# Performance work log

Hardware: AMD Instinct MI355X
Metric: run time of the kernel (lower is better)

## Reference

```python
import jax, jax.numpy as jnp
import numpy as np

HEADS = 8

def setup_inputs() -> dict:
    key = jax.random.key(0)
    ks = jax.random.split(key, 11)
    B, S, E = 4, 2048, 512
    sc = 1.0 / np.sqrt(E)
    return {
        "inputs": jax.random.normal(ks[0], (B, S, E), jnp.float32),
        "entangle": jax.random.uniform(ks[1], (S,), jnp.float32),
        "Wq": jax.random.normal(ks[2], (E, E), jnp.float32) * sc,
        "bq": jax.random.normal(ks[3], (E,), jnp.float32) * 0.01,
        "Wk": jax.random.normal(ks[4], (E, E), jnp.float32) * sc,
        "bk": jax.random.normal(ks[5], (E,), jnp.float32) * 0.01,
        "Wv": jax.random.normal(ks[6], (E, E), jnp.float32) * sc,
        "bv": jax.random.normal(ks[7], (E,), jnp.float32) * 0.01,
        "Wo": jax.random.normal(ks[8], (E, E), jnp.float32) * sc,
        "bo": jax.random.normal(ks[9], (E,), jnp.float32) * 0.01,
    }

def reference(inputs, entangle, Wq, bq, Wk, bk, Wv, bv, Wo, bo):
    B, S, E = inputs.shape
    H = HEADS
    D = E // H
    # torch nn.Linear: y = x @ W.T + b
    Q = (inputs @ Wq.T + bq).reshape(B, S, H, D)
    K = (inputs @ Wk.T + bk).reshape(B, S, H, D)
    V = (inputs @ Wv.T + bv).reshape(B, S, H, D)
    scores = jnp.einsum('bqhd,bkhd->bhqk', Q, K) / jnp.sqrt(jnp.float32(D))
    # entangle broadcast as (1,1,S,1): per-query-position scaling before softmax
    scores = scores * entangle[None, None, :, None]
    attn = jax.nn.softmax(scores, axis=-1)
    out = jnp.einsum('bhqk,bkhd->bqhd', attn, V).reshape(B, S, E)
    return out @ Wo.T + bo
```

## Files before the change

### kernel.cpp

```cpp
#include <hip/hip_runtime.h>
#include <hip/hip_bf16.h>

#define BB 4
#define SS 2048
#define EE 512
#define HH 8
#define DD 64

typedef __attribute__((ext_vector_type(8))) short bf16x8;
typedef __attribute__((ext_vector_type(4))) float f32x4;
typedef __attribute__((ext_vector_type(4))) unsigned int u32x4;

__device__ __forceinline__ unsigned short f2bf(float f) {
    __hip_bfloat16 h = __float2bfloat16(f);
    return *reinterpret_cast<unsigned short*>(&h);
}

__device__ __forceinline__ unsigned int cvtpk(float lo, float hi) {
    unsigned int r;
    asm("v_cvt_pk_bf16_f32 %0, %1, %2" : "=v"(r) : "v"(lo), "v"(hi));
    return r;
}

__device__ __forceinline__ float ex2(float x) {
    float r;
    asm("v_exp_f32 %0, %1" : "=v"(r) : "v"(x));
    return r;
}

__device__ __forceinline__ void pl32(unsigned int& a, unsigned int& b) {
    asm("v_permlane32_swap_b32 %0, %1" : "+v"(a), "+v"(b));
}
__device__ __forceinline__ void pl16(unsigned int& a, unsigned int& b) {
    asm("v_permlane16_swap_b32 %0, %1" : "+v"(a), "+v"(b));
}

__device__ __forceinline__ void gll16(const unsigned short* g, unsigned short* l) {
    __builtin_amdgcn_global_load_lds(
        (const __attribute__((address_space(1))) unsigned int*)g,
        (__attribute__((address_space(3))) unsigned int*)l,
        16, 0, 0);
}

template<typename OutT, bool TRANSPOSE_V, int TM, bool AF32>
__global__ __launch_bounds__(256, 3)
void gemm_mfma_nt(const unsigned short* __restrict__ Abf,
                  const float* __restrict__ Af,
                  const float* __restrict__ W0, const float* __restrict__ b0, OutT* __restrict__ C0,
                  const float* __restrict__ W1, const float* __restrict__ b1, OutT* __restrict__ C1,
                  const float* __restrict__ W2, const float* __restrict__ b2, OutT* __restrict__ C2,
                  const float* __restrict__ rowscale,
                  int M, int N, int K)
{
    const float* W    = (blockIdx.z == 0) ? W0 : (blockIdx.z == 1) ? W1 : W2;
    const float* bias = (blockIdx.z == 0) ? b0 : (blockIdx.z == 1) ? b1 : b2;
    OutT* C           = (blockIdx.z == 0) ? C0 : (blockIdx.z == 1) ? C1 : C2;

    constexpr int MT  = TM / 32;
    constexpr int NA  = TM / 64;
    constexpr int STG = 3 * TM * 32;
    __shared__ unsigned short lds[STG + 3 * 128 * 32];
    unsigned short* As = lds;
    unsigned short* Bs = lds + STG;

    const int tid  = threadIdx.x;
    const int wave = tid >> 6, lane = tid & 63;
    const int quad = lane >> 4, r16 = lane & 15;
    const int m0 = blockIdx.x * TM, n0 = blockIdx.y * 128;
    const int wm0 = (wave >> 1) * (TM / 2), wn0 = (wave & 1) * 64;

    f32x4 acc[MT][4];
    const f32x4 zero = {0.f, 0.f, 0.f, 0.f};
    #pragma unroll
    for (int i = 0; i < MT; ++i)
        #pragma unroll
        for (int j = 0; j < 4; ++j) acc[i][j] = zero;

    const int swz = (r16 >> 1) & 3;

    int acb[NA > 0 ? NA : 1], arow[NA > 0 ? NA : 1], acc_[NA > 0 ? NA : 1];
    #pragma unroll
    for (int j = 0; j < NA; ++j) {
        const int cb = wave * 64 + j * 256, c = cb + lane;
        acb[j] = cb; arow[j] = c >> 2; acc_[j] = (c & 3) ^ ((arow[j] >> 1) & 3);
    }
    int wcb[2], wrow[2], wcc[2];
    #pragma unroll
    for (int j = 0; j < 2; ++j) {
        const int cb = wave * 64 + j * 256, c = cb + lane;
        wcb[j] = cb; wrow[j] = c >> 2; wcc[j] = (c & 3) ^ ((wrow[j] >> 1) & 3);
    }

    f32x4 ra[2 * (NA > 0 ? NA : 1)];
    f32x4 rw[4];

    auto issue = [&](int bi, int k0) {
        if constexpr (AF32) {
            #pragma unroll
            for (int j = 0; j < NA; ++j) {
                const float* p = &Af[(size_t)(m0 + arow[j]) * K + k0 + acc_[j] * 8];
                ra[2 * j]     = *reinterpret_cast<const f32x4*>(p);
                ra[2 * j + 1] = *reinterpret_cast<const f32x4*>(p + 4);
            }
        } else {
            #pragma unroll
            for (int j = 0; j < NA; ++j)
                gll16(&Abf[(size_t)(m0 + arow[j]) * K + k0 + acc_[j] * 8],
                      &As[bi * TM * 32 + acb[j] * 8]);
        }
        #pragma unroll
        for (int j = 0; j < 2; ++j) {
            const float* p = &W[(size_t)(n0 + wrow[j]) * K + k0 + wcc[j] * 8];
            rw[2 * j]     = *reinterpret_cast<const f32x4*>(p);
            rw[2 * j + 1] = *reinterpret_cast<const f32x4*>(p + 4);
        }
    };
    auto commit = [&](int bi) {
        if constexpr (AF32) {
            #pragma unroll
            for (int j = 0; j < NA; ++j) {
                const u32x4 v = {cvtpk(ra[2*j][0], ra[2*j][1]), cvtpk(ra[2*j][2], ra[2*j][3]),
                                 cvtpk(ra[2*j+1][0], ra[2*j+1][1]), cvtpk(ra[2*j+1][2], ra[2*j+1][3])};
                *reinterpret_cast<u32x4*>(&As[bi * TM * 32 + (acb[j] + lane) * 8]) = v;
            }
        }
        #pragma unroll
        for (int j = 0; j < 2; ++j) {
            const u32x4 v = {cvtpk(rw[2*j][0], rw[2*j][1]), cvtpk(rw[2*j][2], rw[2*j][3]),
                             cvtpk(rw[2*j+1][0], rw[2*j+1][1]), cvtpk(rw[2*j+1][2], rw[2*j+1][3])};
            *reinterpret_cast<u32x4*>(&Bs[bi * 128 * 32 + (wcb[j] + lane) * 8]) = v;
        }
    };

    issue(0, 0);
    asm volatile("s_waitcnt vmcnt(0)" ::: "memory");
    commit(0);
    issue(1, 32);

    const int NI = K / 32;
    for (int i = 0; i < NI; ++i) {
        const int cur = i % 3;
        asm volatile("s_waitcnt lgkmcnt(0)" ::: "memory");
        __builtin_amdgcn_s_barrier();
        __builtin_amdgcn_sched_barrier(0);
        if (i + 1 < NI) {
            asm volatile("s_waitcnt vmcnt(0)" ::: "memory");
            commit((i + 1) % 3);
        }
        if (i + 2 < NI) issue((i + 2) % 3, (i + 2) * 32);

        bf16x8 af[MT], bfr[4];
        #pragma unroll
        for (int t = 0; t < MT; ++t)
            af[t]  = *reinterpret_cast<bf16x8*>(&As[cur * TM * 32 + ((wm0 + t * 16 + r16) * 4 + (quad ^ swz)) * 8]);
        #pragma unroll
        for (int t = 0; t < 4; ++t)
            bfr[t] = *reinterpret_cast<bf16x8*>(&Bs[cur * 128 * 32 + ((wn0 + t * 16 + r16) * 4 + (quad ^ swz)) * 8]);
        #pragma unroll
        for (int mt = 0; mt < MT; ++mt)
            #pragma unroll
            for (int nt = 0; nt < 4; ++nt)
                acc[mt][nt] = __builtin_amdgcn_mfma_f32_16x16x32_bf16(
                    af[mt], bfr[nt], acc[mt][nt], 0, 0, 0);
    }

    if (TRANSPOSE_V && blockIdx.z == 2) {
        __syncthreads();
        #pragma unroll
        for (int mt = 0; mt < MT; ++mt) {
            const int s_local = wm0 + mt * 16 + quad * 4;
            #pragma unroll
            for (int nt = 0; nt < 4; ++nt) {
                const int d_local = wn0 + nt * 16 + r16;
                const float bv = bias[n0 + d_local];
                uint2 o;
                o.x = cvtpk(acc[mt][nt][0] + bv, acc[mt][nt][1] + bv);
                o.y = cvtpk(acc[mt][nt][2] + bv, acc[mt][nt][3] + bv);
                *reinterpret_cast<uint2*>(&lds[d_local * 132 + s_local]) = o;
            }
        }
        __syncthreads();
        const int bb = m0 >> 11, s0 = m0 & (SS - 1);
        unsigned short* Vtp = (unsigned short*)C2 + (size_t)bb * EE * SS + s0;
        const int scol = (tid & 15) * 8;
        #pragma unroll
        for (int p = 0; p < 8; ++p) {
            const int row = p * 16 + (tid >> 4);
            const uint2 lo = *reinterpret_cast<const uint2*>(&lds[row * 132 + scol]);
            const uint2 hi = *reinterpret_cast<const uint2*>(&lds[row * 132 + scol + 4]);
            const u32x4 v = {lo.x, lo.y, hi.x, hi.y};
            *reinterpret_cast<u32x4*>(&Vtp[(size_t)(n0 + row) * SS + scol]) = v;
        }
        return;
    }
    if constexpr (sizeof(OutT) == 2) {
        const bool doscale = (rowscale != nullptr) && (blockIdx.z == 0);
        __syncthreads();
        #pragma unroll
        for (int mt = 0; mt < MT; ++mt) {
            float rs[4];
            #pragma unroll
            for (int r = 0; r < 4; ++r) {
                const int row = m0 + wm0 + mt * 16 + quad * 4 + r;
                rs[r] = doscale ? rowscale[row & (SS - 1)] * 0.18033688f : 1.0f;
            }
            #pragma unroll
            for (int nt = 0; nt < 4; ++nt) {
                const int col = wn0 + nt * 16 + r16;
                const float bv = bias[n0 + col];
                #pragma unroll
                for (int r = 0; r < 4; ++r) {
                    const int row = wm0 + mt * 16 + quad * 4 + r;
                    lds[row * 132 + col] = f2bf((acc[mt][nt][r] + bv) * rs[r]);
                }
            }
        }
        __syncthreads();
        const int scol = (tid & 15) * 8;
        #pragma unroll
        for (int p = 0; p < TM / 16; ++p) {
            const int row = p * 16 + (tid >> 4);
            const uint2 lo = *reinterpret_cast<const uint2*>(&lds[row * 132 + scol]);
            const uint2 hi = *reinterpret_cast<const uint2*>(&lds[row * 132 + scol + 4]);
            const u32x4 v = {lo.x, lo.y, hi.x, hi.y};
            *reinterpret_cast<u32x4*>(&((unsigned short*)C)[(size_t)(m0 + row) * N + n0 + scol]) = v;
        }
    } else {
        float* fl = reinterpret_cast<float*>(lds);
        __syncthreads();
        #pragma unroll
        for (int mt = 0; mt < MT; ++mt) {
            #pragma unroll
            for (int nt = 0; nt < 4; ++nt) {
                const int col = wn0 + nt * 16 + r16;
                const float bv = bias[n0 + col];
                #pragma unroll
                for (int r = 0; r < 4; ++r) {
                    const int row = wm0 + mt * 16 + quad * 4 + r;
                    fl[row * 132 + col] = acc[mt][nt][r] + bv;
                }
            }
        }
        __syncthreads();
        const int scol = (tid & 31) * 4;
        #pragma unroll
        for (int p = 0; p < TM / 8; ++p) {
            const int row = p * 8 + (tid >> 5);
            const f32x4 v = *reinterpret_cast<const f32x4*>(&fl[row * 132 + scol]);
            *reinterpret_cast<f32x4*>(&((float*)C)[(size_t)(m0 + row) * N + n0 + scol]) = v;
        }
    }
}

#define QBLK 128
#define KVB  128

__global__ __launch_bounds__(256, 2)
void attn_mfma(const unsigned short* __restrict__ Q,
               const unsigned short* __restrict__ K,
               const unsigned short* __restrict__ Vt,
               unsigned short* __restrict__ O)
{
    __shared__ unsigned short Ks[2][KVB * 64];
    __shared__ unsigned short Vs[2][64 * KVB];

    const int tid  = threadIdx.x;
    const int wave = tid >> 6, lane = tid & 63;
    const int quad = lane >> 4, r16 = lane & 15;
    const int h  = blockIdx.x;
    const int q0 = blockIdx.y * QBLK;
    const int b  = blockIdx.z;
    const size_t base    = (size_t)b * SS * EE + (size_t)h * DD;
    const size_t base_vt = ((size_t)b * HH + h) * DD * SS;

    bf16x8 qf[2][2];
    #pragma unroll
    for (int s = 0; s < 2; ++s) {
        const int qrow = q0 + s * 64 + wave * 16 + r16;
        #pragma unroll
        for (int dh = 0; dh < 2; ++dh)
            qf[s][dh] = *reinterpret_cast<const bf16x8*>(
                &Q[base + (size_t)qrow * EE + dh * 32 + quad * 8]);
    }

    const unsigned short* kp[4];
    const unsigned short* vp[4];
    int cbs[4];
    #pragma unroll
    for (int j = 0; j < 4; ++j) {
        const int cb = wave * 64 + j * 256;
        cbs[j] = cb;
        const int c  = cb + lane;
        const int rowK = c >> 3, ccK = (c & 7) ^ (rowK & 7);
        kp[j] = &K[base + (size_t)rowK * EE + ccK * 8];
        const int rowV = c >> 4, ccV = (c & 15) ^ (rowV & 15);
        vp[j] = &Vt[base_vt + (size_t)rowV * SS + ccV * 8];
    }

    auto stage = [&](int bi, int kt) {
        const size_t ko = (size_t)kt * KVB * EE;
        const int    vo = kt * KVB;
        #pragma unroll
        for (int j = 0; j < 4; ++j) {
            gll16(kp[j] + ko, &Ks[bi][cbs[j] * 8]);
            gll16(vp[j] + vo, &Vs[bi][cbs[j] * 8]);
        }
    };

    float l_lane[2] = {0.f, 0.f};
    f32x4 o_acc[2][4];
    const f32x4 zero = {0.f, 0.f, 0.f, 0.f};
    #pragma unroll
    for (int s = 0; s < 2; ++s)
        #pragma unroll
        for (int dt = 0; dt < 4; ++dt) o_acc[s][dt] = zero;

    const int swz7 = r16 & 7;

    stage(0, 0);

    constexpr int NT = SS / KVB;
    for (int kt = 0; kt < NT; ++kt) {
        const int cur = kt & 1;
        asm volatile("s_waitcnt vmcnt(0)" ::: "memory");
        __builtin_amdgcn_s_barrier();
        __builtin_amdgcn_sched_barrier(0);
        if (kt + 1 < NT) stage(cur ^ 1, kt + 1);

        const unsigned short* Kc = &Ks[cur][0];
        const unsigned short* Vc = &Vs[cur][0];

        f32x4 st[2][8];
        #pragma unroll
        for (int s = 0; s < 2; ++s)
            #pragma unroll
            for (int tn = 0; tn < 8; ++tn) st[s][tn] = zero;
        __builtin_amdgcn_s_setprio(1);
        #pragma unroll
        for (int tn = 0; tn < 8; ++tn) {
            const bf16x8 kf0 = *reinterpret_cast<const bf16x8*>(
                &Kc[((tn * 16 + r16) * 8 + (quad ^ swz7)) * 8]);
            const bf16x8 kf1 = *reinterpret_cast<const bf16x8*>(
                &Kc[((tn * 16 + r16) * 8 + ((quad + 4) ^ swz7)) * 8]);
            #pragma unroll
            for (int s = 0; s < 2; ++s) {
                st[s][tn] = __builtin_amdgcn_mfma_f32_16x16x32_bf16(kf0, qf[s][0], st[s][tn], 0, 0, 0);
                st[s][tn] = __builtin_amdgcn_mfma_f32_16x16x32_bf16(kf1, qf[s][1], st[s][tn], 0, 0, 0);
            }
        }
        __builtin_amdgcn_s_setprio(0);

        bf16x8 pf[2][4];
        #pragma unroll
        for (int s = 0; s < 2; ++s) {
            unsigned int w[8][2];
            #pragma unroll
            for (int tn = 0; tn < 8; ++tn) {
                const float p0 = ex2(st[s][tn][0]);
                const float p1 = ex2(st[s][tn][1]);
                const float p2 = ex2(st[s][tn][2]);
                const float p3 = ex2(st[s][tn][3]);
                l_lane[s] += (p0 + p1) + (p2 + p3);
                w[tn][0] = cvtpk(p0, p1);
                w[tn][1] = cvtpk(p2, p3);
            }
            #pragma unroll
            for (int j = 0; j < 4; ++j) {
                unsigned int a0 = w[2 * j][0], a2 = w[2 * j + 1][0];
                pl32(a0, a2); pl16(a0, a2);
                unsigned int a1 = w[2 * j][1], a3 = w[2 * j + 1][1];
                pl32(a1, a3); pl16(a1, a3);
                const u32x4 u = {a0, a1, a2, a3};
                pf[s][j] = __builtin_bit_cast(bf16x8, u);
            }
        }

        __builtin_amdgcn_s_setprio(1);
        #pragma unroll
        for (int j = 0; j < 4; ++j) {
            #pragma unroll
            for (int dt = 0; dt < 4; ++dt) {
                const bf16x8 vf = *reinterpret_cast<const bf16x8*>(
                    &Vc[((dt * 16 + r16) * 16 + ((4 * j + quad) ^ r16)) * 8]);
                o_acc[0][dt] = __builtin_amdgcn_mfma_f32_16x16x32_bf16(pf[0][j], vf, o_acc[0][dt], 0, 0, 0);
                o_acc[1][dt] = __builtin_amdgcn_mfma_f32_16x16x32_bf16(pf[1][j], vf, o_acc[1][dt], 0, 0, 0);
            }
        }
        __builtin_amdgcn_s_setprio(0);
    }

    float lq[2];
    #pragma unroll
    for (int s = 0; s < 2; ++s) {
        float l = l_lane[s];
        l += __shfl_xor(l, 16, 64);
        l += __shfl_xor(l, 32, 64);
        lq[s] = l;
    }

    unsigned short* ob = &Ks[0][0];
    __syncthreads();
    #pragma unroll
    for (int s = 0; s < 2; ++s) {
        #pragma unroll
        for (int r = 0; r < 4; ++r) {
            const float il = 1.0f / __shfl(lq[s], quad * 4 + r, 64);
            const int ql = s * 64 + wave * 16 + quad * 4 + r;
            #pragma unroll
            for (int dt = 0; dt < 4; ++dt)
                ob[ql * 68 + dt * 16 + r16] = f2bf(o_acc[s][dt][r] * il);
        }
    }
    __syncthreads();
    const int orow = tid >> 3, ocol = (tid & 7) * 8;
    #pragma unroll
    for (int p = 0; p < 4; ++p) {
        const int ql = p * 32 + orow;
        const uint2 lo = *reinterpret_cast<const uint2*>(&ob[ql * 68 + ocol]);
        const uint2 hi = *reinterpret_cast<const uint2*>(&ob[ql * 68 + ocol + 4]);
        const u32x4 v = {lo.x, lo.y, hi.x, hi.y};
        *reinterpret_cast<u32x4*>(&O[base + (size_t)(q0 + ql) * EE + ocol]) = v;
    }
}

extern "C" void kernel_launch(void* const* d_in, const int* in_sizes, int n_in,
                              void* d_out, int out_size, void* d_ws, size_t ws_size,
                              hipStream_t stream) {
    const float* x   = (const float*)d_in[0];
    const float* ent = (const float*)d_in[1];
    const float* Wq  = (const float*)d_in[2];
    const float* bq  = (const float*)d_in[3];
    const float* Wk  = (const float*)d_in[4];
    const float* bk  = (const float*)d_in[5];
    const float* Wv  = (const float*)d_in[6];
    const float* bv  = (const float*)d_in[7];
    const float* Wo  = (const float*)d_in[8];
    const float* bo  = (const float*)d_in[9];
    float* out = (float*)d_out;

    const size_t n_x = (size_t)BB * SS * EE;
    const size_t n_w = (size_t)EE * EE;

    unsigned short* xb  = (unsigned short*)d_ws;
    unsigned short* wqb = xb + n_x;
    unsigned short* wkb = wqb + n_w;
    unsigned short* wvb = wkb + n_w;
    unsigned short* wob = wvb + n_w;
    unsigned short* Qb  = wob + n_w;
    unsigned short* Kb  = Qb + n_x;
    unsigned short* Vtb = Kb + n_x;
    unsigned short* AOb = Vtb + n_x;

    const int M = BB * SS;

    dim3 gq(M / 128, EE / 128, 3);
    gemm_mfma_nt<unsigned short, true, 128, true><<<gq, 256, 0, stream>>>(
        nullptr, x, Wq, bq, Qb, Wk, bk, Kb, Wv, bv, Vtb, ent, M, EE, EE);

    dim3 ga(HH, SS / QBLK, BB);
    attn_mfma<<<ga, 256, 0, stream>>>(Qb, Kb, Vtb, AOb);

    dim3 go(M / 64, EE / 128, 1);
    gemm_mfma_nt<float, false, 64, false><<<go, 256, 0, stream>>>(
        AOb, nullptr, Wo, bo, out, Wo, bo, out, Wo, bo, out, nullptr, M, EE, EE);
}
```

Measured before the change: 156.2 us.

## Fuse Q/K/V projections into one kernel sharing the x tile

Replaces the z-batched QKV GEMM, which used 128-row tiles and reloaded and converted the fp32 input once per projection, with a dedicated kernel. Each block loads a 64-row x tile once and computes all three projections against it, using double buffering. The goal is to cut input reads and fp32-to-bf16 conversions by three times. In exchange, each thread holds three times as many accumulators, which raises register pressure and risks occupancy. The output GEMM is specialised into a simpler non-templated kernel.

```diff
diff --git a/kernel.cpp b/kernel.cpp
--- a/kernel.cpp
+++ b/kernel.cpp
@@ -42,22 +42,190 @@
         16, 0, 0);
 }
 
-template<typename OutT, bool TRANSPOSE_V, int TM, bool AF32>
+__global__ __launch_bounds__(256, 2)
+void qkv_fused(const float* __restrict__ x,
+               const float* __restrict__ Wq, const float* __restrict__ bq, unsigned short* __restrict__ Qb,
+               const float* __restrict__ Wk, const float* __restrict__ bk, unsigned short* __restrict__ Kb,
+               const float* __restrict__ Wv, const float* __restrict__ bv, unsigned short* __restrict__ Vtb,
+               const float* __restrict__ ent)
+{
+    constexpr int K   = EE;
+    constexpr int N   = EE;
+    constexpr int ASZ = 64 * 32;
+    constexpr int BSZ = 128 * 32;
+    constexpr int BUF = ASZ + 3 * BSZ;
+    __shared__ unsigned short lds[2 * BUF];
+
+    const int tid  = threadIdx.x;
+    const int wave = tid >> 6, lane = tid & 63;
+    const int quad = lane >> 4, r16 = lane & 15;
+    const int m0 = blockIdx.x * 64, n0 = blockIdx.y * 128;
+    const int wm0 = (wave >> 1) * 32, wn0 = (wave & 1) * 64;
+
+    const float* Ws[3] = {Wq, Wk, Wv};
+
+    f32x4 acc[3][2][4];
+    const f32x4 zero = {0.f, 0.f, 0.f, 0.f};
+    #pragma unroll
+    for (int o = 0; o < 3; ++o)
+        #pragma unroll
+        for (int mt = 0; mt < 2; ++mt)
+            #pragma unroll
+            for (int nt = 0; nt < 4; ++nt) acc[o][mt][nt] = zero;
+
+    const int swz = (r16 >> 1) & 3;
+
+    const int cbA = wave * 64, cA = cbA + lane;
+    const int rowA = cA >> 2, ccA = (cA & 3) ^ ((rowA >> 1) & 3);
+    int wcb[2], wrow[2], wcc[2];
+    #pragma unroll
+    for (int j = 0; j < 2; ++j) {
+        const int cb = wave * 64 + j * 256, c = cb + lane;
+        wcb[j] = cb; wrow[j] = c >> 2; wcc[j] = (c & 3) ^ ((wrow[j] >> 1) & 3);
+    }
+
+    f32x4 ra[2];
+    f32x4 rw[3][2][2];
+
+    auto issue = [&](int k0) {
+        const float* pa = &x[(size_t)(m0 + rowA) * K + k0 + ccA * 8];
+        ra[0] = *reinterpret_cast<const f32x4*>(pa);
+        ra[1] = *reinterpret_cast<const f32x4*>(pa + 4);
+        #pragma unroll
+        for (int o = 0; o < 3; ++o)
+            #pragma unroll
+            for (int j = 0; j < 2; ++j) {
+                const float* p = &Ws[o][(size_t)(n0 + wrow[j]) * K + k0 + wcc[j] * 8];
+                rw[o][j][0] = *reinterpret_cast<const f32x4*>(p);
+                rw[o][j][1] = *reinterpret_cast<const f32x4*>(p + 4);
+            }
+    };
+    auto commit = [&](int bi) {
+        unsigned short* As = lds + bi * BUF;
+        const u32x4 va = {cvtpk(ra[0][0], ra[0][1]), cvtpk(ra[0][2], ra[0][3]),
+                          cvtpk(ra[1][0], ra[1][1]), cvtpk(ra[1][2], ra[1][3])};
+        *reinterpret_cast<u32x4*>(&As[(cbA + lane) * 8]) = va;
+        #pragma unroll
+        for (int o = 0; o < 3; ++o) {
+            unsigned short* Bo = lds + bi * BUF + ASZ + o * BSZ;
+            #pragma unroll
+            for (int j = 0; j < 2; ++j) {
+                const u32x4 v = {cvtpk(rw[o][j][0][0], rw[o][j][0][1]), cvtpk(rw[o][j][0][2], rw[o][j][0][3]),
+                                 cvtpk(rw[o][j][1][0], rw[o][j][1][1]), cvtpk(rw[o][j][1][2], rw[o][j][1][3])};
+                *reinterpret_cast<u32x4*>(&Bo[(wcb[j] + lane) * 8]) = v;
+            }
+        }
+    };
+
+    issue(0);
+    asm volatile("s_waitcnt vmcnt(0)" ::: "memory");
+    commit(0);
+    issue(32);
+
+    constexpr int NI = K / 32;
+    for (int i = 0; i < NI; ++i) {
+        const int cur = i & 1;
+        asm volatile("s_waitcnt lgkmcnt(0)" ::: "memory");
+        __builtin_amdgcn_s_barrier();
+        __builtin_amdgcn_sched_barrier(0);
+        if (i + 1 < NI) {
+            asm volatile("s_waitcnt vmcnt(0)" ::: "memory");
+            commit(cur ^ 1);
+        }
+        if (i + 2 < NI) issue((i + 2) * 32);
+
+        const unsigned short* As = lds + cur * BUF;
+        bf16x8 af[2];
+        #pragma unroll
+        for (int t = 0; t < 2; ++t)
+            af[t] = *reinterpret_cast<const bf16x8*>(
+                &As[((wm0 + t * 16 + r16) * 4 + (quad ^ swz)) * 8]);
+        #pragma unroll
+        for (int o = 0; o < 3; ++o) {
+            const unsigned short* Bo = lds + cur * BUF + ASZ + o * BSZ;
+            bf16x8 bfr[4];
+            #pragma unroll
+            for (int t = 0; t < 4; ++t)
+                bfr[t] = *reinterpret_cast<const bf16x8*>(
+                    &Bo[((wn0 + t * 16 + r16) * 4 + (quad ^ swz)) * 8]);
+            #pragma unroll
+            for (int mt = 0; mt < 2; ++mt)
+                #pragma unroll
+                for (int nt = 0; nt < 4; ++nt)
+                    acc[o][mt][nt] = __builtin_amdgcn_mfma_f32_16x16x32_bf16(
+                        af[mt], bfr[nt], acc[o][mt][nt], 0, 0, 0);
+        }
+    }
+
+    #pragma unroll
+    for (int o = 0; o < 2; ++o) {
+        const float* bias = (o == 0) ? bq : bk;
+        unsigned short* dst = (o == 0) ? Qb : Kb;
+        __syncthreads();
+        #pragma unroll
+        for (int mt = 0; mt < 2; ++mt) {
+            float rs[4];
+            #pragma unroll
+            for (int r = 0; r < 4; ++r) {
+                const int grow = m0 + wm0 + mt * 16 + quad * 4 + r;
+                rs[r] = (o == 0) ? ent[grow & (SS - 1)] * 0.18033688f : 1.0f;
+            }
+            #pragma unroll
+            for (int nt = 0; nt < 4; ++nt) {
+                const int col = wn0 + nt * 16 + r16;
+                const float bvv = bias[n0 + col];
+                #pragma unroll
+                for (int r = 0; r < 4; ++r) {
+                    const int row = wm0 + mt * 16 + quad * 4 + r;
+                    lds[row * 132 + col] = f2bf((acc[o][mt][nt][r] + bvv) * rs[r]);
+                }
+            }
+        }
+        __syncthreads();
+        const int scol = (tid & 15) * 8;
+        #pragma unroll
+        for (int p = 0; p < 4; ++p) {
+            const int row = p * 16 + (tid >> 4);
+            const uint2 lo = *reinterpret_cast<const uint2*>(&lds[row * 132 + scol]);
+            const uint2 hi = *reinterpret_cast<const uint2*>(&lds[row * 132 + scol + 4]);
+            const u32x4 v = {lo.x, lo.y, hi.x, hi.y};
+            *reinterpret_cast<u32x4*>(&dst[(size_t)(m0 + row) * N + n0 + scol]) = v;
+        }
+    }
+    __syncthreads();
+    #pragma unroll
+    for (int mt = 0; mt < 2; ++mt) {
+        const int s_local = wm0 + mt * 16 + quad * 4;
+        #pragma unroll
+        for (int nt = 0; nt < 4; ++nt) {
+            const int d_local = wn0 + nt * 16 + r16;
+            const float bvv = bv[n0 + d_local];
+            uint2 o2;
+            o2.x = cvtpk(acc[2][mt][nt][0] + bvv, acc[2][mt][nt][1] + bvv);
+            o2.y = cvtpk(acc[2][mt][nt][2] + bvv, acc[2][mt][nt][3] + bvv);
+            *reinterpret_cast<uint2*>(&lds[d_local * 68 + s_local]) = o2;
+        }
+    }
+    __syncthreads();
+    const int bb = m0 >> 11, s0 = m0 & (SS - 1);
+    unsigned short* Vtp = Vtb + (size_t)bb * EE * SS + s0;
+    const int ocol = (tid & 7) * 8;
+    #pragma unroll
+    for (int p = 0; p < 4; ++p) {
+        const int d = p * 32 + (tid >> 3);
+        const uint2 lo = *reinterpret_cast<const uint2*>(&lds[d * 68 + ocol]);
+        const uint2 hi = *reinterpret_cast<const uint2*>(&lds[d * 68 + ocol + 4]);
+        const u32x4 v = {lo.x, lo.y, hi.x, hi.y};
+        *reinterpret_cast<u32x4*>(&Vtp[(size_t)(n0 + d) * SS + ocol]) = v;
+    }
+}
+
 __global__ __launch_bounds__(256, 3)
-void gemm_mfma_nt(const unsigned short* __restrict__ Abf,
-                  const float* __restrict__ Af,
-                  const float* __restrict__ W0, const float* __restrict__ b0, OutT* __restrict__ C0,
-                  const float* __restrict__ W1, const float* __restrict__ b1, OutT* __restrict__ C1,
-                  const float* __restrict__ W2, const float* __restrict__ b2, OutT* __restrict__ C2,
-                  const float* __restrict__ rowscale,
-                  int M, int N, int K)
+void gemm_out(const unsigned short* __restrict__ Abf,
+              const float* __restrict__ W, const float* __restrict__ bias,
+              float* __restrict__ C, int M, int N, int K)
 {
-    const float* W    = (blockIdx.z == 0) ? W0 : (blockIdx.z == 1) ? W1 : W2;
-    const float* bias = (blockIdx.z == 0) ? b0 : (blockIdx.z == 1) ? b1 : b2;
-    OutT* C           = (blockIdx.z == 0) ? C0 : (blockIdx.z == 1) ? C1 : C2;
-
-    constexpr int MT  = TM / 32;
-    constexpr int NA  = TM / 64;
+    constexpr int TM = 64;
     constexpr int STG = 3 * TM * 32;
     __shared__ unsigned short lds[STG + 3 * 128 * 32];
     unsigned short* As = lds;
@@ -69,45 +237,27 @@
     const int m0 = blockIdx.x * TM, n0 = blockIdx.y * 128;
     const int wm0 = (wave >> 1) * (TM / 2), wn0 = (wave & 1) * 64;
 
-    f32x4 acc[MT][4];
+    f32x4 acc[2][4];
     const f32x4 zero = {0.f, 0.f, 0.f, 0.f};
     #pragma unroll
-    for (int i = 0; i < MT; ++i)
+    for (int i = 0; i < 2; ++i)
         #pragma unroll
         for (int j = 0; j < 4; ++j) acc[i][j] = zero;
 
     const int swz = (r16 >> 1) & 3;
 
-    int acb[NA > 0 ? NA : 1], arow[NA > 0 ? NA : 1], acc_[NA > 0 ? NA : 1];
-    #pragma unroll
-    for (int j = 0; j < NA; ++j) {
-        const int cb = wave * 64 + j * 256, c = cb + lane;
-        acb[j] = cb; arow[j] = c >> 2; acc_[j] = (c & 3) ^ ((arow[j] >> 1) & 3);
-    }
+    const int cbA = wave * 64, cA = cbA + lane;
+    const int rowA = cA >> 2, ccA = (cA & 3) ^ ((rowA >> 1) & 3);
     int wcb[2], wrow[2], wcc[2];
     #pragma unroll
     for (int j = 0; j < 2; ++j) {
         const int cb = wave * 64 + j * 256, c = cb + lane;
         wcb[j] = cb; wrow[j] = c >> 2; wcc[j] = (c & 3) ^ ((wrow[j] >> 1) & 3);
     }
-
-    f32x4 ra[2 * (NA > 0 ? NA : 1)];
     f32x4 rw[4];
 
     auto issue = [&](int bi, int k0) {
-        if constexpr (AF32) {
-            #pragma unroll
-            for (int j = 0; j < NA; ++j) {
-                const float* p = &Af[(size_t)(m0 + arow[j]) * K + k0 + acc_[j] * 8];
-                ra[2 * j]     = *reinterpret_cast<const f32x4*>(p);
-                ra[2 * j + 1] = *reinterpret_cast<const f32x4*>(p + 4);
-            }
-        } else {
-            #pragma unroll
-            for (int j = 0; j < NA; ++j)
-                gll16(&Abf[(size_t)(m0 + arow[j]) * K + k0 + acc_[j] * 8],
-                      &As[bi * TM * 32 + acb[j] * 8]);
-        }
+        gll16(&Abf[(size_t)(m0 + rowA) * K + k0 + ccA * 8], &As[bi * TM * 32 + cbA * 8]);
         #pragma unroll
         for (int j = 0; j < 2; ++j) {
             const float* p = &W[(size_t)(n0 + wrow[j]) * K + k0 + wcc[j] * 8];
@@ -116,14 +266,6 @@
         }
     };
     auto commit = [&](int bi) {
-        if constexpr (AF32) {
-            #pragma unroll
-            for (int j = 0; j < NA; ++j) {
-                const u32x4 v = {cvtpk(ra[2*j][0], ra[2*j][1]), cvtpk(ra[2*j][2], ra[2*j][3]),
-                                 cvtpk(ra[2*j+1][0], ra[2*j+1][1]), cvtpk(ra[2*j+1][2], ra[2*j+1][3])};
-                *reinterpret_cast<u32x4*>(&As[bi * TM * 32 + (acb[j] + lane) * 8]) = v;
-            }
-        }
         #pragma unroll
         for (int j = 0; j < 2; ++j) {
             const u32x4 v = {cvtpk(rw[2*j][0], rw[2*j][1]), cvtpk(rw[2*j][2], rw[2*j][3]),
@@ -149,106 +291,43 @@
         }
         if (i + 2 < NI) issue((i + 2) % 3, (i + 2) * 32);
 
-        bf16x8 af[MT], bfr[4];
-        #pragma unroll
-        for (int t = 0; t < MT; ++t)
+        bf16x8 af[2], bfr[4];
+        #pragma unroll
+        for (int t = 0; t < 2; ++t)
             af[t]  = *reinterpret_cast<bf16x8*>(&As[cur * TM * 32 + ((wm0 + t * 16 + r16) * 4 + (quad ^ swz)) * 8]);
         #pragma unroll
         for (int t = 0; t < 4; ++t)
             bfr[t] = *reinterpret_cast<bf16x8*>(&Bs[cur * 128 * 32 + ((wn0 + t * 16 + r16) * 4 + (quad ^ swz)) * 8]);
         #pragma unroll
-        for (int mt = 0; mt < MT; ++mt)
+        for (int mt = 0; mt < 2; ++mt)
             #pragma unroll
             for (int nt = 0; nt < 4; ++nt)
                 acc[mt][nt] = __builtin_amdgcn_mfma_f32_16x16x32_bf16(
                     af[mt], bfr[nt], acc[mt][nt], 0, 0, 0);
     }
 
-    if (TRANSPOSE_V && blockIdx.z == 2) {
-        __syncthreads();
-        #pragma unroll
-        for (int mt = 0; mt < MT; ++mt) {
-            const int s_local = wm0 + mt * 16 + quad * 4;
-            #pragma unroll
-            for (int nt = 0; nt < 4; ++nt) {
-                const int d_local = wn0 + nt * 16 + r16;
-                const float bv = bias[n0 + d_local];
-                uint2 o;
-                o.x = cvtpk(acc[mt][nt][0] + bv, acc[mt][nt][1] + bv);
-                o.y = cvtpk(acc[mt][nt][2] + bv, acc[mt][nt][3] + bv);
-                *reinterpret_cast<uint2*>(&lds[d_local * 132 + s_local]) = o;
-            }
-        }
-        __syncthreads();
-        const int bb = m0 >> 11, s0 = m0 & (SS - 1);
-        unsigned short* Vtp = (unsigned short*)C2 + (size_t)bb * EE * SS + s0;
-        const int scol = (tid & 15) * 8;
-        #pragma unroll
-        for (int p = 0; p < 8; ++p) {
-            const int row = p * 16 + (tid >> 4);
-            const uint2 lo = *reinterpret_cast<const uint2*>(&lds[row * 132 + scol]);
-            const uint2 hi = *reinterpret_cast<const uint2*>(&lds[row * 132 + scol + 4]);
-            const u32x4 v = {lo.x, lo.y, hi.x, hi.y};
-            *reinterpret_cast<u32x4*>(&Vtp[(size_t)(n0 + row) * SS + scol]) = v;
-        }
-        return;
-    }
-    if constexpr (sizeof(OutT) == 2) {
-        const bool doscale = (rowscale != nullptr) && (blockIdx.z == 0);
-        __syncthreads();
-        #pragma unroll
-        for (int mt = 0; mt < MT; ++mt) {
-            float rs[4];
+    float* fl = reinterpret_cast<float*>(lds);
+    __syncthreads();
+    #pragma unroll
+    for (int mt = 0; mt < 2; ++mt) {
+        #pragma unroll
+        for (int nt = 0; nt < 4; ++nt) {
+            const int col = wn0 + nt * 16 + r16;
+            const float bvv = bias[n0 + col];
             #pragma unroll
             for (int r = 0; r < 4; ++r) {
-                const int row = m0 + wm0 + mt * 16 + quad * 4 + r;
-                rs[r] = doscale ? rowscale[row & (SS - 1)] * 0.18033688f : 1.0f;
-            }
-            #pragma unroll
-            for (int nt = 0; nt < 4; ++nt) {
-                const int col = wn0 + nt * 16 + r16;
-                const float bv = bias[n0 + col];
-                #pragma unroll
-                for (int r = 0; r < 4; ++r) {
-                    const int row = wm0 + mt * 16 + quad * 4 + r;
-                    lds[row * 132 + col] = f2bf((acc[mt][nt][r] + bv) * rs[r]);
-                }
-            }
-        }
-        __syncthreads();
-        const int scol = (tid & 15) * 8;
-        #pragma unroll
-        for (int p = 0; p < TM / 16; ++p) {
-            const int row = p * 16 + (tid >> 4);
-            const uint2 lo = *reinterpret_cast<const uint2*>(&lds[row * 132 + scol]);
-            const uint2 hi = *reinterpret_cast<const uint2*>(&lds[row * 132 + scol + 4]);
-            const u32x4 v = {lo.x, lo.y, hi.x, hi.y};
-            *reinterpret_cast<u32x4*>(&((unsigned short*)C)[(size_t)(m0 + row) * N + n0 + scol]) = v;
-        }
-    } else {
-        float* fl = reinterpret_cast<float*>(lds);
-        __syncthreads();
-        #pragma unroll
-        for (int mt = 0; mt < MT; ++mt) {
-            #pragma unroll
-            for (int nt = 0; nt < 4; ++nt) {
-                const int col = wn0 + nt * 16 + r16;
-                const float bv = bias[n0 + col];
-                #pragma unroll
-                for (int r = 0; r < 4; ++r) {
-                    const int row = wm0 + mt * 16 + quad * 4 + r;
-                    fl[row * 132 + col] = acc[mt][nt][r] + bv;
-                }
-            }
-        }
-        __syncthreads();
-        const int scol = (tid & 31) * 4;
-        #pragma unroll
-        for (int p = 0; p < TM / 8; ++p) {
-            const int row = p * 8 + (tid >> 5);
-            const f32x4 v = *reinterpret_cast<const f32x4*>(&fl[row * 132 + scol]);
-            *reinterpret_cast<f32x4*>(&((float*)C)[(size_t)(m0 + row) * N + n0 + scol]) = v;
-        }
+                const int row = wm0 + mt * 16 + quad * 4 + r;
+                fl[row * 132 + col] = acc[mt][nt][r] + bvv;
+            }
+        }
+    }
+    __syncthreads();
+    const int scol = (tid & 31) * 4;
+    #pragma unroll
+    for (int p = 0; p < 8; ++p) {
+        const int row = p * 8 + (tid >> 5);
+        const f32x4 v = *reinterpret_cast<const f32x4*>(&fl[row * 132 + scol]);
+        *reinterpret_cast<f32x4*>(&C[(size_t)(m0 + row) * N + n0 + scol]) = v;
     }
 }
 
@@ -453,14 +532,12 @@
 
     const int M = BB * SS;
 
-    dim3 gq(M / 128, EE / 128, 3);
-    gemm_mfma_nt<unsigned short, true, 128, true><<<gq, 256, 0, stream>>>(
-        nullptr, x, Wq, bq, Qb, Wk, bk, Kb, Wv, bv, Vtb, ent, M, EE, EE);
+    dim3 gq(M / 64, EE / 128, 1);
+    qkv_fused<<<gq, 256, 0, stream>>>(x, Wq, bq, Qb, Wk, bk, Kb, Wv, bv, Vtb, ent);
 
     dim3 ga(HH, SS / QBLK, BB);
     attn_mfma<<<ga, 256, 0, stream>>>(Qb, Kb, Vtb, AOb);
 
     dim3 go(M / 64, EE / 128, 1);
-    gemm_mfma_nt<float, false, 64, false><<<go, 256, 0, stream>>>(
-        AOb, nullptr, Wo, bo, out, Wo, bo, out, Wo, bo, out, nullptr, M, EE, EE);
-}
+    gemm_out<<<go, 256, 0, stream>>>(AOb, Wo, bo, out, M, EE, EE);
+}
```

After: 159.1 us. No clear change (+1.9%).

## Add dedicated output-projection GEMM with BK=64 triple-buffered LDS pipeline

Applied to the files above, without the earlier changes.

Replaces the generic templated GEMM used for the output projection with a specialized kernel. It processes K in 64-wide steps split into two 32-wide sub-tiles and keeps three LDS buffers, so global loads are issued two iterations ahead. The fp32 weights are held in registers and converted to bf16 before being written to LDS. This halves the number of barriers per K and deepens prefetch, at the cost of more LDS and more registers, which may reduce occupancy. The output projection is a small share of total time, which is dominated by attention.

```diff
diff --git a/kernel.cpp b/kernel.cpp
--- a/kernel.cpp
+++ b/kernel.cpp
@@ -249,6 +249,130 @@
             const f32x4 v = *reinterpret_cast<const f32x4*>(&fl[row * 132 + scol]);
             *reinterpret_cast<f32x4*>(&((float*)C)[(size_t)(m0 + row) * N + n0 + scol]) = v;
         }
+    }
+}
+
+__global__ __launch_bounds__(256, 2)
+void gemm_out_bk64(const unsigned short* __restrict__ Abf,
+                   const float* __restrict__ W, const float* __restrict__ bias,
+                   float* __restrict__ C, int M, int N, int K)
+{
+    constexpr int TM  = 64;
+    constexpr int ASB = TM * 32;
+    constexpr int BSB = 128 * 32;
+    __shared__ unsigned short lds[3 * 2 * ASB + 3 * 2 * BSB];
+    unsigned short* As = lds;
+    unsigned short* Bs = lds + 3 * 2 * ASB;
+
+    const int tid  = threadIdx.x;
+    const int wave = tid >> 6, lane = tid & 63;
+    const int quad = lane >> 4, r16 = lane & 15;
+    const int m0 = blockIdx.x * TM, n0 = blockIdx.y * 128;
+    const int wm0 = (wave >> 1) * 32, wn0 = (wave & 1) * 64;
+
+    f32x4 acc[2][4];
+    const f32x4 zero = {0.f, 0.f, 0.f, 0.f};
+    #pragma unroll
+    for (int i = 0; i < 2; ++i)
+        #pragma unroll
+        for (int j = 0; j < 4; ++j) acc[i][j] = zero;
+
+    const int swz = (r16 >> 1) & 3;
+
+    const int cbA = wave * 64, cA = cbA + lane;
+    const int rowA = cA >> 2, ccA = (cA & 3) ^ ((rowA >> 1) & 3);
+    int wcb[2], wrow[2], wcc[2];
+    #pragma unroll
+    for (int j = 0; j < 2; ++j) {
+        const int cb = wave * 64 + j * 256, c = cb + lane;
+        wcb[j] = cb; wrow[j] = c >> 2; wcc[j] = (c & 3) ^ ((wrow[j] >> 1) & 3);
+    }
+    f32x4 rw[2][2][2];
+
+    auto issue = [&](int bi, int k0) {
+        #pragma unroll
+        for (int s = 0; s < 2; ++s) {
+            const int ks = k0 + s * 32;
+            gll16(&Abf[(size_t)(m0 + rowA) * K + ks + ccA * 8],
+                  &As[(bi * 2 + s) * ASB + cbA * 8]);
+            #pragma unroll
+            for (int j = 0; j < 2; ++j) {
+                const float* p = &W[(size_t)(n0 + wrow[j]) * K + ks + wcc[j] * 8];
+                rw[s][j][0] = *reinterpret_cast<const f32x4*>(p);
+                rw[s][j][1] = *reinterpret_cast<const f32x4*>(p + 4);
+            }
+        }
+    };
+    auto commit = [&](int bi) {
+        #pragma unroll
+        for (int s = 0; s < 2; ++s)
+            #pragma unroll
+            for (int j = 0; j < 2; ++j) {
+                const u32x4 v = {cvtpk(rw[s][j][0][0], rw[s][j][0][1]), cvtpk(rw[s][j][0][2], rw[s][j][0][3]),
+                                 cvtpk(rw[s][j][1][0], rw[s][j][1][1]), cvtpk(rw[s][j][1][2], rw[s][j][1][3])};
+                *reinterpret_cast<u32x4*>(&Bs[(bi * 2 + s) * BSB + (wcb[j] + lane) * 8]) = v;
+            }
+    };
+
+    issue(0, 0);
+    asm volatile("s_waitcnt vmcnt(0)" ::: "memory");
+    commit(0);
+    issue(1, 64);
+
+    const int NI = K / 64;
+    for (int i = 0; i < NI; ++i) {
+        const int cur = i % 3;
+        asm volatile("s_waitcnt lgkmcnt(0)" ::: "memory");
+        __builtin_amdgcn_s_barrier();
+        __builtin_amdgcn_sched_barrier(0);
+        if (i + 1 < NI) {
+            asm volatile("s_waitcnt vmcnt(0)" ::: "memory");
+            commit((i + 1) % 3);
+        }
+        if (i + 2 < NI) issue((i + 2) % 3, (i + 2) * 64);
+
+        #pragma unroll
+        for (int s = 0; s < 2; ++s) {
+            const unsigned short* Asub = &As[(cur * 2 + s) * ASB];
+            const unsigned short* Bsub = &Bs[(cur * 2 + s) * BSB];
+            bf16x8 af[2], bfr[4];
+            #pragma unroll
+            for (int t = 0; t < 2; ++t)
+                af[t]  = *reinterpret_cast<const bf16x8*>(&Asub[((wm0 + t * 16 + r16) * 4 + (quad ^ swz)) * 8]);
+            #pragma unroll
+            for (int t = 0; t < 4; ++t)
+                bfr[t] = *reinterpret_cast<const bf16x8*>(&Bsub[((wn0 + t * 16 + r16) * 4 + (quad ^ swz)) * 8]);
+            #pragma unroll
+            for (int mt = 0; mt < 2; ++mt)
+                #pragma unroll
+                for (int nt = 0; nt < 4; ++nt)
+                    acc[mt][nt] = __builtin_amdgcn_mfma_f32_16x16x32_bf16(
+                        af[mt], bfr[nt], acc[mt][nt], 0, 0, 0);
+        }
+    }
+
+    float* fl = reinterpret_cast<float*>(lds);
+    __syncthreads();
+    #pragma unroll
+    for (int mt = 0; mt < 2; ++mt) {
+        #pragma unroll
+        for (int nt = 0; nt < 4; ++nt) {
+            const int col = wn0 + nt * 16 + r16;
+            const float bvv = bias[n0 + col];
+            #pragma unroll
+            for (int r = 0; r < 4; ++r) {
+                const int row = wm0 + mt * 16 + quad * 4 + r;
+                fl[row * 132 + col] = acc[mt][nt][r] + bvv;
+            }
+        }
+    }
+    __syncthreads();
+    const int scol = (tid & 31) * 4;
+    #pragma unroll
+    for (int p = 0; p < 8; ++p) {
+        const int row = p * 8 + (tid >> 5);
+        const f32x4 v = *reinterpret_cast<const f32x4*>(&fl[row * 132 + scol]);
+        *reinterpret_cast<f32x4*>(&C[(size_t)(m0 + row) * N + n0 + scol]) = v;
     }
 }
 
@@ -461,6 +585,5 @@
     attn_mfma<<<ga, 256, 0, stream>>>(Qb, Kb, Vtb, AOb);
 
     dim3 go(M / 64, EE / 128, 1);
-    gemm_mfma_nt<float, false, 64, false><<<go, 256, 0, stream>>>(
-        AOb, nullptr, Wo, bo, out, Wo, bo, out, Wo, bo, out, nullptr, M, EE, EE);
-}
+    gemm_out_bk64<<<go, 256, 0, stream>>>(AOb, Wo, bo, out, M, EE, EE);
+}
```

After: 154.8 us. Within noise of the previous version (-0.9%).
